# Optimization experiments

Measured on AMD Instinct MI355X. Metric: run time of the kernel, lower is better.

## Reference

```python
import jax, jax.numpy as jnp
import numpy as np

HEAD_DIM = 64
EMB_DIM = 1024
BATCH = 4
SEQ = 4096


def setup_inputs() -> dict:
    key = jax.random.key(0)
    kx, kq, kk, kv = jax.random.split(key, 4)
    scale = 1.0 / np.sqrt(EMB_DIM)
    x = jax.random.normal(kx, (BATCH, SEQ, EMB_DIM), dtype=jnp.float32)
    # nn.Linear(emb_dim, head_dim, bias=False): weight [head_dim, emb_dim]; store transposed [emb_dim, head_dim]
    Wq = jax.random.normal(kq, (EMB_DIM, HEAD_DIM), dtype=jnp.float32) * scale
    Wk = jax.random.normal(kk, (EMB_DIM, HEAD_DIM), dtype=jnp.float32) * scale
    Wv = jax.random.normal(kv, (EMB_DIM, HEAD_DIM), dtype=jnp.float32) * scale
    return {"x": x, "Wq": Wq, "Wk": Wk, "Wv": Wv}


def reference(x, Wq, Wk, Wv):
    # x: [b, s, e] -> q,k,v: [b, s, d]
    q = jnp.einsum("bse,ed->bsd", x, Wq)
    k = jnp.einsum("bse,ed->bsd", x, Wk)
    v = jnp.einsum("bse,ed->bsd", x, Wv)
    d = q.shape[-1]
    # scores: [b, s, s], scaled by 1/sqrt(head_dim)
    scores = jnp.einsum("bqd,bkd->bqk", q, k) / jnp.sqrt(jnp.asarray(d, q.dtype))
    s = x.shape[1]
    causal = jnp.tril(jnp.ones((s, s), dtype=bool))
    scores = jnp.where(causal, scores, jnp.asarray(-jnp.inf, scores.dtype))
    attn = jax.nn.softmax(scores, axis=-1)
    return jnp.einsum("bqk,bkd->bqd", attn, v)
```

## Files before the change

kernel.cpp:

```cpp
#include <hip/hip_runtime.h>
#include <hip/hip_bf16.h>
#include <math.h>

#define BATCH 4
#define SEQ   4096
#define EMB   1024
#define HD    64

#define QBLK  64
#define KBLK  64
#define CHUNK 512
#define BM    32

#define NSPB  288
#define NSLOT (BATCH * NSPB)

#define SCL   0.1803368801111204f

typedef _Float16 half8 __attribute__((ext_vector_type(8)));
typedef _Float16 half4 __attribute__((ext_vector_type(4)));
typedef float    f32x4 __attribute__((ext_vector_type(4)));

#define GLOAD_LDS16(g, l) __builtin_amdgcn_global_load_lds(                 \
    (const __attribute__((address_space(1))) void*)(g),                     \
    (__attribute__((address_space(3))) void*)(l), 16, 0, 0)

static __device__ __forceinline__ float bf2f(unsigned int u16) {
    union { unsigned int i; float f; } v;
    v.i = u16 << 16;
    return v.f;
}

__global__ void detect_dtype(const unsigned short* __restrict__ x,
                             int* __restrict__ flag)
{
    const int tid = threadIdx.x;
    int big = 0;
    for (int i = tid; i < 2048; i += 64) {
        const int e = (x[i] >> 7) & 0xff;
        if (e > 146) big++;
    }
    #pragma unroll
    for (int off = 32; off; off >>= 1) big += __shfl_xor(big, off);
    if (tid == 0) *flag = (big > 200) ? 0 : 1;
}

__global__ __launch_bounds__(256) void w_to_fp16t(
    const void* __restrict__ Wqp, const void* __restrict__ Wkp,
    const void* __restrict__ Wvp, const int* __restrict__ flagp,
    _Float16* __restrict__ Wt)
{
    const int gid = blockIdx.x * 256 + threadIdx.x;
    const int n   = gid >> 7;
    const int kc  = (gid & 127) << 3;
    const int mat = n >> 6, d = n & 63;
    const void* Wp = (mat == 0) ? Wqp : (mat == 1 ? Wkp : Wvp);

    half8 o;
    if (*flagp) {
        const unsigned short* W = (const unsigned short*)Wp;
        #pragma unroll
        for (int j = 0; j < 8; ++j) o[j] = (_Float16)bf2f(W[(kc + j) * HD + d]);
    } else {
        const float* W = (const float*)Wp;
        #pragma unroll
        for (int j = 0; j < 8; ++j) o[j] = (_Float16)W[(kc + j) * HD + d];
    }
    *(half8*)&Wt[n * EMB + kc] = o;
}

__global__ __launch_bounds__(256) void qkv_gemm(
    const void* __restrict__ xp, const _Float16* __restrict__ Wt,
    const int* __restrict__ flagp,
    _Float16* __restrict__ Qh, _Float16* __restrict__ Kh,
    _Float16* __restrict__ Vth)
{
    __shared__ _Float16 Xs[2][BM * 64];

    const int tid  = threadIdx.x;
    const int w    = tid >> 6;
    const int lane = tid & 63;
    const int c15  = lane & 15;
    const int kg   = lane >> 4;
    const size_t row0 = (size_t)blockIdx.x * BM;
    const int isbf = *flagp;

    const int sr = tid >> 3, ss = tid & 7;
    const size_t gbase = (row0 + sr) * EMB + ss * 8;
    const int lidx = sr * 64 + ((ss ^ (sr & 7)) << 3);

    float4 f0[2], f1[2];
    uint4  u0,    u1;

    auto ldc = [&](int t, float4* f, uint4* u) {
        if (isbf) *u = *(const uint4*)((const unsigned short*)xp + gbase + t * 64);
        else {
            f[0] = *(const float4*)((const float*)xp + gbase + t * 64);
            f[1] = *(const float4*)((const float*)xp + gbase + t * 64 + 4);
        }
    };
    auto wrc = [&](int buf, const float4* f, const uint4* u) {
        half8 h;
        if (isbf) {
            const unsigned int uu[4] = {u->x, u->y, u->z, u->w};
            #pragma unroll
            for (int q = 0; q < 4; ++q) {
                h[2 * q]     = (_Float16)bf2f(uu[q] & 0xffffu);
                h[2 * q + 1] = (_Float16)bf2f(uu[q] >> 16);
            }
        } else {
            const float ff[8] = {f[0].x, f[0].y, f[0].z, f[0].w,
                                 f[1].x, f[1].y, f[1].z, f[1].w};
            #pragma unroll
            for (int q = 0; q < 8; ++q) h[q] = (_Float16)ff[q];
        }
        *(half8*)&Xs[buf][lidx] = h;
    };

    f32x4 acc[2][3];
    #pragma unroll
    for (int mf = 0; mf < 2; ++mf)
        #pragma unroll
        for (int nf = 0; nf < 3; ++nf) acc[mf][nf] = (f32x4){0.f, 0.f, 0.f, 0.f};

    ldc(0, f0, &u0);
    wrc(0, f0, &u0);
    int cur = 0;

    for (int t = 0; t < 16; ++t) {
        if (t + 1 < 16) ldc(t + 1, f1, &u1);
        __syncthreads();

        #pragma unroll
        for (int kk = 0; kk < 2; ++kk) {
            half8 a[2], b[3];
            #pragma unroll
            for (int mf = 0; mf < 2; ++mf) {
                const int R = mf * 16 + c15;
                a[mf] = *(const half8*)&Xs[cur][R * 64 +
                        (((kk * 4 + kg) ^ (R & 7)) << 3)];
            }
            #pragma unroll
            for (int nf = 0; nf < 3; ++nf) {
                const int n = w * 48 + nf * 16 + c15;
                b[nf] = *(const half8*)&Wt[n * EMB + t * 64 + kk * 32 + kg * 8];
            }
            #pragma unroll
            for (int mf = 0; mf < 2; ++mf)
                #pragma unroll
                for (int nf = 0; nf < 3; ++nf)
                    acc[mf][nf] = __builtin_amdgcn_mfma_f32_16x16x32_f16(
                        a[mf], b[nf], acc[mf][nf], 0, 0, 0);
        }

        if (t + 1 < 16) wrc(cur ^ 1, f1, &u1);
        cur ^= 1;
    }

    #pragma unroll
    for (int nf = 0; nf < 3; ++nf) {
        const int nc  = w * 48 + nf * 16;
        const int mat = nc >> 6;
        const int d   = (nc & 63) + c15;
        if (mat < 2) {
            _Float16* Out = mat ? Kh : Qh;
            #pragma unroll
            for (int mf = 0; mf < 2; ++mf)
                #pragma unroll
                for (int r = 0; r < 4; ++r)
                    Out[(row0 + mf * 16 + kg * 4 + r) * HD + d] =
                        (_Float16)acc[mf][nf][r];
        } else {
            const int bb = (int)(row0 >> 12);
            const int s0 = (int)(row0 & 4095);
            #pragma unroll
            for (int mf = 0; mf < 2; ++mf) {
                half4 hv;
                #pragma unroll
                for (int r = 0; r < 4; ++r) hv[r] = (_Float16)acc[mf][nf][r];
                *(half4*)&Vth[((size_t)bb * HD + d) * SEQ + s0 + mf * 16 + kg * 4] = hv;
            }
        }
    }
}

__global__ __launch_bounds__(256) void attn_split(
    const _Float16* __restrict__ Qh, const _Float16* __restrict__ Kh,
    const _Float16* __restrict__ Vth,
    _Float16* __restrict__ PoG, float* __restrict__ PmG,
    float* __restrict__ PlG)
{
    __shared__ _Float16 Kt[2][KBLK * HD];
    __shared__ _Float16 Vt[2][HD * KBLK];
    __shared__ _Float16 Ps[4][16 * KBLK];

    const int b = blockIdx.y;
    const int f = blockIdx.x;
    int c = 0, off = 0, cnt = 64;
    while (f >= off + cnt) { off += cnt; ++c; cnt -= 8; }
    const int qb = 8 * c + (f - off);
    const int q0 = qb * QBLK;
    const int kstart = c * CHUNK;
    const int kend   = min(kstart + CHUNK, q0 + QBLK);
    const int nt     = (kend - kstart) / KBLK;

    const int tid  = threadIdx.x;
    const int w    = tid >> 6;
    const int lane = tid & 63;
    const int col  = lane & 15;
    const int kg   = lane >> 4;

    const size_t bo = (size_t)b * SEQ;
    const _Float16* Kb = Kh + bo * HD;
    const _Float16* Vb = Vth + (size_t)b * HD * SEQ;

    const _Float16* Qp = Qh + (bo + q0 + w * 16 + col) * HD;
    const half8 aq0 = *(const half8*)(Qp + kg * 8);
    const half8 aq1 = *(const half8*)(Qp + 32 + kg * 8);

    f32x4 O[4];
    float mreg[4], lreg[4];
    #pragma unroll
    for (int cq = 0; cq < 4; ++cq) O[cq] = (f32x4){0.f, 0.f, 0.f, 0.f};
    #pragma unroll
    for (int r = 0; r < 4; ++r) { mreg[r] = -INFINITY; lreg[r] = 0.f; }

    const int wh = w & 1;
    auto stage = [&](int t, int buf) {
        const int k0 = kstart + t * KBLK;
        if (w < 2) {
            const _Float16* g = Kb + (size_t)k0 * HD;
            #pragma unroll
            for (int i = 0; i < 4; ++i) {
                const int c2 = (wh * 4 + i) * 64 + lane;
                const int key = c2 >> 3, slot = c2 & 7;
                GLOAD_LDS16(g + key * HD + ((slot ^ (key & 7)) << 3),
                            &Kt[buf][(wh * 4 + i) * 512]);
            }
        } else {
            const _Float16* g = Vb + k0;
            #pragma unroll
            for (int i = 0; i < 4; ++i) {
                const int c2 = (wh * 4 + i) * 64 + lane;
                const int dim = c2 >> 3, slot = c2 & 7;
                GLOAD_LDS16(g + (size_t)dim * SEQ + ((slot ^ (dim & 7)) << 3),
                            &Vt[buf][(wh * 4 + i) * 512]);
            }
        }
    };

    stage(0, 0);
    int cur = 0;

    for (int t = 0; t < nt; ++t) {
        __syncthreads();
        if (t + 1 < nt) stage(t + 1, cur ^ 1);

        const int k0 = kstart + t * KBLK;

        f32x4 S[4];
        #pragma unroll
        for (int cq = 0; cq < 4; ++cq) {
            const int key = cq * 16 + col;
            const int sw  = key & 7;
            const half8 bk0 = *(const half8*)&Kt[cur][(key * 8 + (kg ^ sw)) * 8];
            const half8 bk1 = *(const half8*)&Kt[cur][(key * 8 + ((4 + kg) ^ sw)) * 8];
            f32x4 acc = (f32x4){0.f, 0.f, 0.f, 0.f};
            acc = __builtin_amdgcn_mfma_f32_16x16x32_f16(aq0, bk0, acc, 0, 0, 0);
            acc = __builtin_amdgcn_mfma_f32_16x16x32_f16(aq1, bk1, acc, 0, 0, 0);
            S[cq] = acc;
        }

        const int rowb  = q0 + w * 16 + kg * 4;
        const bool full = (k0 + KBLK - 1) <= (q0 + w * 16);
        float p[4][4];
        #pragma unroll
        for (int cq = 0; cq < 4; ++cq) {
            const int key = k0 + cq * 16 + col;
            #pragma unroll
            for (int r = 0; r < 4; ++r) {
                float s = S[cq][r] * SCL;
                if (!full && key > rowb + r) s = -INFINITY;
                p[cq][r] = s;
            }
        }

        float alpha[4];
        #pragma unroll
        for (int r = 0; r < 4; ++r) {
            float v = fmaxf(fmaxf(p[0][r], p[1][r]), fmaxf(p[2][r], p[3][r]));
            v = fmaxf(v, __shfl_xor(v, 1));
            v = fmaxf(v, __shfl_xor(v, 2));
            v = fmaxf(v, __shfl_xor(v, 4));
            v = fmaxf(v, __shfl_xor(v, 8));
            const float mn = fmaxf(mreg[r], v);
            alpha[r] = exp2f(mreg[r] - mn);
            mreg[r]  = mn;
        }

        #pragma unroll
        for (int cq = 0; cq < 4; ++cq) {
            const int colidx = cq * 16 + col;
            #pragma unroll
            for (int r = 0; r < 4; ++r) {
                const float pv = exp2f(p[cq][r] - mreg[r]);
                p[cq][r] = pv;
                const int row = kg * 4 + r;
                Ps[w][row * 64 + (colidx ^ ((row & 7) << 3))] = (_Float16)pv;
            }
        }
        #pragma unroll
        for (int r = 0; r < 4; ++r) {
            float v = (p[0][r] + p[1][r]) + (p[2][r] + p[3][r]);
            v += __shfl_xor(v, 1);
            v += __shfl_xor(v, 2);
            v += __shfl_xor(v, 4);
            v += __shfl_xor(v, 8);
            lreg[r] = lreg[r] * alpha[r] + v;
        }

        #pragma unroll
        for (int cq = 0; cq < 4; ++cq)
            #pragma unroll
            for (int r = 0; r < 4; ++r)
                O[cq][r] *= alpha[r];

        #pragma unroll
        for (int s2 = 0; s2 < 2; ++s2) {
            const int prow = col;
            const half8 pa = *(const half8*)&Ps[w][prow * 64 +
                ((s2 * 32 + kg * 8) ^ ((prow & 7) << 3))];
            #pragma unroll
            for (int cq = 0; cq < 4; ++cq) {
                const int dim = cq * 16 + col;
                const half8 bv = *(const half8*)&Vt[cur][(dim * 8 +
                    ((s2 * 4 + kg) ^ (dim & 7))) * 8];
                O[cq] = __builtin_amdgcn_mfma_f32_16x16x32_f16(pa, bv, O[cq], 0, 0, 0);
            }
        }
        cur ^= 1;
    }

    const int pslot = b * NSPB + f;
    #pragma unroll
    for (int cq = 0; cq < 4; ++cq)
        #pragma unroll
        for (int r = 0; r < 4; ++r) {
            const int rloc = w * 16 + kg * 4 + r;
            PoG[((size_t)pslot * 64 + rloc) * 64 + cq * 16 + col] =
                (_Float16)O[cq][r];
        }
    if (col == 0) {
        #pragma unroll
        for (int r = 0; r < 4; ++r) {
            const int rloc = w * 16 + kg * 4 + r;
            PmG[pslot * 64 + rloc] = mreg[r];
            PlG[pslot * 64 + rloc] = lreg[r];
        }
    }
}

__global__ __launch_bounds__(128) void attn_merge(
    const _Float16* __restrict__ PoG, const float* __restrict__ PmG,
    const float* __restrict__ PlG, const int* __restrict__ flagp,
    void* __restrict__ outp)
{
    const int qb   = blockIdx.x;
    const int b    = blockIdx.y;
    const int rg   = blockIdx.z;
    const int nc   = (qb >> 3) + 1;
    const int tid  = threadIdx.x;
    const int rloc = rg * 16 + (tid >> 3);
    const int d0   = (tid & 7) * 8;
    const int isbf = *flagp;

    float mm = -INFINITY;
    for (int i = 0; i < nc; ++i) {
        const int sl = b * NSPB + i * (68 - 4 * i) + qb - 8 * i;
        mm = fmaxf(mm, PmG[sl * 64 + rloc]);
    }
    float acc[8] = {0.f, 0.f, 0.f, 0.f, 0.f, 0.f, 0.f, 0.f};
    float ls = 0.f;
    for (int i = 0; i < nc; ++i) {
        const int sl = b * NSPB + i * (68 - 4 * i) + qb - 8 * i;
        const float wsc = exp2f(PmG[sl * 64 + rloc] - mm);
        const half8 po = *(const half8*)&PoG[((size_t)sl * 64 + rloc) * 64 + d0];
        #pragma unroll
        for (int j = 0; j < 8; ++j) acc[j] += wsc * (float)po[j];
        ls += wsc * PlG[sl * 64 + rloc];
    }
    const float il = 1.f / ls;
    const size_t obase = ((size_t)b * SEQ + qb * QBLK + rloc) * HD + d0;
    if (isbf) {
        __hip_bfloat16* Ob = (__hip_bfloat16*)outp;
        #pragma unroll
        for (int j = 0; j < 8; ++j) Ob[obase + j] = __float2bfloat16(acc[j] * il);
    } else {
        float* Of = (float*)outp;
        #pragma unroll
        for (int j = 0; j < 8; ++j) Of[obase + j] = acc[j] * il;
    }
}

extern "C" void kernel_launch(void* const* d_in, const int* in_sizes, int n_in,
                              void* d_out, int out_size, void* d_ws, size_t ws_size,
                              hipStream_t stream)
{
    const void* x  = d_in[0];
    const void* Wq = d_in[1];
    const void* Wk = d_in[2];
    const void* Wv = d_in[3];

    const size_t N = (size_t)BATCH * SEQ * HD;
    int*      flag = (int*)d_ws;
    _Float16* Qh   = (_Float16*)((char*)d_ws + 256);
    _Float16* Kh   = Qh + N;
    _Float16* Vth  = Kh + N;
    _Float16* Wt   = Vth + N;
    float*    PmG  = (float*)(Wt + 192 * 1024);
    float*    PlG  = PmG + (size_t)NSLOT * 64;
    _Float16* PoG  = (_Float16*)(PlG + (size_t)NSLOT * 64);

    detect_dtype<<<1, 64, 0, stream>>>((const unsigned short*)x, flag);

    w_to_fp16t<<<96, 256, 0, stream>>>(Wq, Wk, Wv, flag, Wt);

    qkv_gemm<<<BATCH * SEQ / BM, 256, 0, stream>>>(x, Wt, flag, Qh, Kh, Vth);

    attn_split<<<dim3(NSPB, BATCH), 256, 0, stream>>>(Qh, Kh, Vth,
                                                      PoG, PmG, PlG);

    attn_merge<<<dim3(SEQ / QBLK, BATCH, 4), 128, 0, stream>>>(PoG, PmG, PlG,
                                                               flag, d_out);
}
```

Measured before the change: 182.0 us.

## Add lazy softmax rescaling, DPP reductions, MFMA priority and unrolled projection pipeline

The attention loop now rescales the O accumulator and running max only when some row's block max exceeds the stored max by more than 4 in the log2 domain, skipping per-tile alpha multiplies in the common case. Row max and sum reductions use DPP lane permutes instead of __shfl_xor. MFMA sections are wrapped in s_setprio to favour matrix issue. The QKV projection loop is unrolled by two with fixed LDS buffers and separate register staging, giving more overlap between global loads and compute. Lazy rescaling lets intermediate exp values reach up to 16 before rescale, which is safe in fp16 but adds a wave-wide vote and a branch.

Result: faster. 174.1 us (-4.3%).

```diff
diff --git a/kernel.cpp b/kernel.cpp
--- a/kernel.cpp
+++ b/kernel.cpp
@@ -24,6 +24,9 @@
 #define GLOAD_LDS16(g, l) __builtin_amdgcn_global_load_lds(                 \
     (const __attribute__((address_space(1))) void*)(g),                     \
     (__attribute__((address_space(3))) void*)(l), 16, 0, 0)
+
+#define DPPF(v, ctrl) __int_as_float(__builtin_amdgcn_update_dpp(           \
+    0, __float_as_int(v), ctrl, 0xF, 0xF, true))
 
 static __device__ __forceinline__ float bf2f(unsigned int u16) {
     union { unsigned int i; float f; } v;
@@ -123,21 +126,14 @@
         #pragma unroll
         for (int nf = 0; nf < 3; ++nf) acc[mf][nf] = (f32x4){0.f, 0.f, 0.f, 0.f};
 
-    ldc(0, f0, &u0);
-    wrc(0, f0, &u0);
-    int cur = 0;
-
-    for (int t = 0; t < 16; ++t) {
-        if (t + 1 < 16) ldc(t + 1, f1, &u1);
-        __syncthreads();
-
+    auto compute = [&](int buf, int t) {
         #pragma unroll
         for (int kk = 0; kk < 2; ++kk) {
             half8 a[2], b[3];
             #pragma unroll
             for (int mf = 0; mf < 2; ++mf) {
                 const int R = mf * 16 + c15;
-                a[mf] = *(const half8*)&Xs[cur][R * 64 +
+                a[mf] = *(const half8*)&Xs[buf][R * 64 +
                         (((kk * 4 + kg) ^ (R & 7)) << 3)];
             }
             #pragma unroll
@@ -152,9 +148,21 @@
                     acc[mf][nf] = __builtin_amdgcn_mfma_f32_16x16x32_f16(
                         a[mf], b[nf], acc[mf][nf], 0, 0, 0);
         }
-
-        if (t + 1 < 16) wrc(cur ^ 1, f1, &u1);
-        cur ^= 1;
+    };
+
+    ldc(0, f0, &u0);
+    wrc(0, f0, &u0);
+    ldc(1, f1, &u1);
+
+    for (int tt = 0; tt < 16; tt += 2) {
+        __syncthreads();
+        if (tt + 2 < 16) ldc(tt + 2, f0, &u0);
+        compute(0, tt);
+        wrc(1, f1, &u1);
+        __syncthreads();
+        if (tt + 3 < 16) ldc(tt + 3, f1, &u1);
+        compute(1, tt + 1);
+        if (tt + 2 < 16) wrc(0, f0, &u0);
     }
 
     #pragma unroll
@@ -259,6 +267,7 @@
         const int k0 = kstart + t * KBLK;
 
         f32x4 S[4];
+        __builtin_amdgcn_s_setprio(1);
         #pragma unroll
         for (int cq = 0; cq < 4; ++cq) {
             const int key = cq * 16 + col;
@@ -270,6 +279,7 @@
             acc = __builtin_amdgcn_mfma_f32_16x16x32_f16(aq1, bk1, acc, 0, 0, 0);
             S[cq] = acc;
         }
+        __builtin_amdgcn_s_setprio(0);
 
         const int rowb  = q0 + w * 16 + kg * 4;
         const bool full = (k0 + KBLK - 1) <= (q0 + w * 16);
@@ -285,17 +295,33 @@
             }
         }
 
-        float alpha[4];
+        float vmax[4];
         #pragma unroll
         for (int r = 0; r < 4; ++r) {
             float v = fmaxf(fmaxf(p[0][r], p[1][r]), fmaxf(p[2][r], p[3][r]));
-            v = fmaxf(v, __shfl_xor(v, 1));
-            v = fmaxf(v, __shfl_xor(v, 2));
-            v = fmaxf(v, __shfl_xor(v, 4));
-            v = fmaxf(v, __shfl_xor(v, 8));
-            const float mn = fmaxf(mreg[r], v);
-            alpha[r] = exp2f(mreg[r] - mn);
-            mreg[r]  = mn;
+            v = fmaxf(v, DPPF(v, 0xB1));
+            v = fmaxf(v, DPPF(v, 0x4E));
+            v = fmaxf(v, DPPF(v, 0x141));
+            v = fmaxf(v, DPPF(v, 0x140));
+            vmax[r] = v;
+        }
+
+        bool grow = false;
+        #pragma unroll
+        for (int r = 0; r < 4; ++r) grow |= (vmax[r] > mreg[r] + 4.0f);
+        float alpha[4] = {1.f, 1.f, 1.f, 1.f};
+        if (__any(grow)) {
+            #pragma unroll
+            for (int r = 0; r < 4; ++r) {
+                const float mn = fmaxf(mreg[r], vmax[r]);
+                alpha[r] = exp2f(mreg[r] - mn);
+                mreg[r]  = mn;
+            }
+            #pragma unroll
+            for (int cq = 0; cq < 4; ++cq)
+                #pragma unroll
+                for (int r = 0; r < 4; ++r)
+                    O[cq][r] *= alpha[r];
         }
 
         #pragma unroll
@@ -312,19 +338,14 @@
         #pragma unroll
         for (int r = 0; r < 4; ++r) {
             float v = (p[0][r] + p[1][r]) + (p[2][r] + p[3][r]);
-            v += __shfl_xor(v, 1);
-            v += __shfl_xor(v, 2);
-            v += __shfl_xor(v, 4);
-            v += __shfl_xor(v, 8);
+            v += DPPF(v, 0xB1);
+            v += DPPF(v, 0x4E);
+            v += DPPF(v, 0x141);
+            v += DPPF(v, 0x140);
             lreg[r] = lreg[r] * alpha[r] + v;
         }
 
-        #pragma unroll
-        for (int cq = 0; cq < 4; ++cq)
-            #pragma unroll
-            for (int r = 0; r < 4; ++r)
-                O[cq][r] *= alpha[r];
-
+        __builtin_amdgcn_s_setprio(1);
         #pragma unroll
         for (int s2 = 0; s2 < 2; ++s2) {
             const int prow = col;
@@ -338,6 +359,7 @@
                 O[cq] = __builtin_amdgcn_mfma_f32_16x16x32_f16(pa, bv, O[cq], 0, 0, 0);
             }
         }
+        __builtin_amdgcn_s_setprio(0);
         cur ^= 1;
     }
 
```
